# Optimization experiments

Hardware: AMD Instinct MI355X
Metric: run time of the kernel (lower is better)

## Reference

```python
import jax, jax.numpy as jnp
import numpy as np

B, N = 1, 512
C_S, C_Z, C_HID, H, P_Q, P_V = 384, 128, 16, 12, 4, 8
W_C = (2.0 / (9.0 * P_Q)) ** 0.5
W_L = (1.0 / 3.0) ** 0.5
F_IN = H * C_Z + H * C_HID + H * P_V * 3 + H * P_V  # 2112


def setup_inputs() -> dict:
    key = jax.random.key(0)
    ks = jax.random.split(key, 14)
    s_i = jax.random.normal(ks[0], (B, N, C_S), jnp.float32)
    z_ij = jax.random.normal(ks[1], (B, N, N, C_Z), jnp.float32)
    # proper rotation matrices via QR so invert_apply is a true rigid inverse
    rot, _ = jnp.linalg.qr(jax.random.normal(ks[2], (B, N, 3, 3), jnp.float32))
    trans = jax.random.normal(ks[3], (B, N, 3), jnp.float32)
    sc = lambda fan: 1.0 / np.sqrt(fan)
    Wq = jax.random.normal(ks[4], (C_S, H, C_HID), jnp.float32) * sc(C_S)
    Wk = jax.random.normal(ks[5], (C_S, H, C_HID), jnp.float32) * sc(C_S)
    Wv = jax.random.normal(ks[6], (C_S, H, C_HID), jnp.float32) * sc(C_S)
    Wqp = jax.random.normal(ks[7], (C_S, H, P_Q, 3), jnp.float32) * sc(C_S)
    Wkp = jax.random.normal(ks[8], (C_S, H, P_Q, 3), jnp.float32) * sc(C_S)
    Wvp = jax.random.normal(ks[9], (C_S, H, P_V, 3), jnp.float32) * sc(C_S)
    Wb = jax.random.normal(ks[10], (C_Z, H), jnp.float32) * sc(C_Z)
    gamma = jax.random.normal(ks[11], (H,), jnp.float32)
    Wf = jax.random.normal(ks[12], (F_IN, C_S), jnp.float32) * sc(F_IN)
    bf = jnp.zeros((C_S,), jnp.float32)
    return {"s_i": s_i, "z_ij": z_ij, "rot": rot, "trans": trans,
            "Wq": Wq, "Wk": Wk, "Wv": Wv, "Wqp": Wqp, "Wkp": Wkp, "Wvp": Wvp,
            "Wb": Wb, "gamma": gamma, "Wf": Wf, "bf": bf}


def _apply(rot, trans, p):
    # rigid transform per residue: R_i @ p + t_i ; p: (B,N,H,P,3)
    return jnp.einsum('bimn,bihpn->bihpm', rot, p) + trans[:, :, None, None, :]


def reference(s_i, z_ij, rot, trans, Wq, Wk, Wv, Wqp, Wkp, Wvp, Wb, gamma, Wf, bf):
    q = jnp.einsum('bic,chd->bihd', s_i, Wq)            # (B,N,H,C_HID)
    k = jnp.einsum('bic,chd->bihd', s_i, Wk)
    v = jnp.einsum('bic,chd->bihd', s_i, Wv)
    qp = jnp.einsum('bic,chpx->bihpx', s_i, Wqp)        # (B,N,H,Pq,3)
    kp = jnp.einsum('bic,chpx->bihpx', s_i, Wkp)
    vp = jnp.einsum('bic,chpx->bihpx', s_i, Wvp)        # (B,N,H,Pv,3)
    b_ij = jnp.einsum('bijc,ch->bijh', z_ij, Wb)        # pair bias (B,N,N,H)

    qp_g = _apply(rot, trans, qp)
    kp_g = _apply(rot, trans, kp)
    # squared global point distances, summed over points: (B,N,N,H)
    d2 = jnp.sum((qp_g[:, :, None] - kp_g[:, None]) ** 2, axis=(-1, -2))

    qk = jnp.einsum('bihd,bjhd->bijh', q, k) * (1.0 / np.sqrt(C_HID))
    logits = W_L * (qk + b_ij - (W_C * 0.5) * gamma * d2)
    a = jax.nn.softmax(logits, axis=2)                  # softmax over j

    o_pair = jnp.einsum('bijh,bijc->bihc', a, z_ij)     # (B,N,H,C_Z)
    o_sc = jnp.einsum('bijh,bjhd->bihd', a, v)          # (B,N,H,C_HID)
    vp_g = _apply(rot, trans, vp)
    o_pt_g = jnp.einsum('bijh,bjhpx->bihpx', a, vp_g)   # (B,N,H,Pv,3)
    # invert_apply at residue i: R_i^T @ (x - t_i)
    o_pt = jnp.einsum('bimn,bihpm->bihpn', rot, o_pt_g - trans[:, :, None, None, :])
    o_norm = jnp.sqrt(jnp.sum(o_pt ** 2, axis=-1) + 1e-12)  # (B,N,H,Pv)

    feat = jnp.concatenate([o_pair.reshape(B, N, -1), o_sc.reshape(B, N, -1),
                            o_pt.reshape(B, N, -1), o_norm.reshape(B, N, -1)], axis=-1)
    return feat @ Wf + bf
```

## Files before the change

### kernel.cpp

```cpp
#include <hip/hip_runtime.h>
#include <hip/hip_bf16.h>
#include <math.h>

#define Nn    512
#define CS    384
#define CZ    128
#define CH    16
#define Hh    12
#define PQ    4
#define PV    8
#define NCOL  1152
#define FIN   2112

#define W_C   0.23570226039551584f
#define W_L   0.5773502691896258f

typedef unsigned short ushort_t;
typedef unsigned int uint_t;
typedef __attribute__((ext_vector_type(8))) short bf16x8;
typedef __attribute__((ext_vector_type(4))) float f32x4;

#define OFF_P      0u
#define OFF_MQ     589824u
#define OFF_MK     595968u
#define OFF_VT     602112u
#define OFF_VPT    651264u
#define OFF_S16    1830912u
#define OFF_WCT    1929216u
#define OFF_WFT    2150400u
#define OFF_F16    2555904u
#define OFF_PP     3145728u
#define OFF_VFRAG  5328896u
#define OFF_EXT    5451776u
#define OFF_EKB    21755904u
#define OFF_EQB    21854208u
#define OFF_WBF    21952512u

__device__ inline ushort_t f2bf(float f) {
  __hip_bfloat16 h = __float2bfloat16(f);
  return *reinterpret_cast<ushort_t*>(&h);
}
__device__ inline float bf2f(ushort_t u) {
  unsigned int x = ((unsigned int)u) << 16;
  return __uint_as_float(x);
}

__global__ __launch_bounds__(384) void k_conv(
    const float* __restrict__ s, const float* __restrict__ Wq,
    const float* __restrict__ Wk, const float* __restrict__ Wv,
    const float* __restrict__ Wqp, const float* __restrict__ Wkp,
    const float* __restrict__ Wvp, const float* __restrict__ Wf,
    const float* __restrict__ Wb,
    ushort_t* __restrict__ s16, ushort_t* __restrict__ WcatT,
    ushort_t* __restrict__ WfT, ushort_t* __restrict__ wbf) {
  int b = blockIdx.x;
  if (b < 512) {
    int idx = b * 384 + threadIdx.x;
    s16[idx] = f2bf(s[idx]);
  } else if (b < 1664) {
    int col = b - 512, k = threadIdx.x;
    float v;
    if      (col < 192)  v = Wq [k * 192 + col];
    else if (col < 384)  v = Wk [k * 192 + col - 192];
    else if (col < 576)  v = Wv [k * 192 + col - 384];
    else if (col < 720)  v = Wqp[k * 144 + col - 576];
    else if (col < 864)  v = Wkp[k * 144 + col - 720];
    else                 v = Wvp[k * 288 + col - 864];
    WcatT[(size_t)col * CS + k] = f2bf(v);
  } else if (b < 2048) {
    int o = b - 1664;
    for (int f = threadIdx.x; f < FIN; f += 384)
      WfT[(size_t)o * FIN + f] = f2bf(Wf[(size_t)f * CS + o]);
  } else {
    int t = threadIdx.x;
    if (t < 256) {
      int kk = t >> 6, l = t & 63;
      int h = l & 15, lk = l >> 4;
#pragma unroll
      for (int e = 0; e < 8; ++e) {
        int c = kk * 32 + lk * 8 + e;
        wbf[t * 8 + e] = (h < Hh) ? f2bf(Wb[c * Hh + h]) : (ushort_t)0;
      }
    }
  }
}

__global__ __launch_bounds__(64) void k_projm(
    const ushort_t* __restrict__ s16, const ushort_t* __restrict__ WcatT,
    float* __restrict__ P) {
  int colt = blockIdx.x;
  int i0 = blockIdx.y * 16;
  int l = threadIdx.x;
  int cl = l & 15, lk = l >> 4;
  f32x4 accA = {0.f, 0.f, 0.f, 0.f}, accB = {0.f, 0.f, 0.f, 0.f};
  const ushort_t* arow = s16 + (size_t)(i0 + cl) * CS;
  const ushort_t* brow = WcatT + (size_t)(colt * 16 + cl) * CS;
#pragma unroll
  for (int kk = 0; kk < 12; kk += 2) {
    bf16x8 a0 = *(const bf16x8*)(arow + kk * 32 + lk * 8);
    bf16x8 b0 = *(const bf16x8*)(brow + kk * 32 + lk * 8);
    accA = __builtin_amdgcn_mfma_f32_16x16x32_bf16(a0, b0, accA, 0, 0, 0);
    bf16x8 a1 = *(const bf16x8*)(arow + (kk + 1) * 32 + lk * 8);
    bf16x8 b1 = *(const bf16x8*)(brow + (kk + 1) * 32 + lk * 8);
    accB = __builtin_amdgcn_mfma_f32_16x16x32_bf16(a1, b1, accB, 0, 0, 0);
  }
#pragma unroll
  for (int r = 0; r < 4; ++r)
    P[(size_t)(i0 + lk * 4 + r) * NCOL + colt * 16 + cl] = accA[r] + accB[r];
}

__global__ __launch_bounds__(64) void k_prep(
    const float* __restrict__ P, const float* __restrict__ rot,
    const float* __restrict__ trans, const float* __restrict__ gamma,
    ushort_t* __restrict__ eqb, ushort_t* __restrict__ ekb,
    float* __restrict__ mq, float* __restrict__ mk,
    ushort_t* __restrict__ vT, ushort_t* __restrict__ vpT) {
  int gid = blockIdx.x * 64 + threadIdx.x;
  int i = gid / Hh, h = gid % Hh;
  const float* Pi = P + (size_t)i * NCOL;
  float R[9], T[3];
#pragma unroll
  for (int m = 0; m < 9; ++m) R[m] = rot[i * 9 + m];
#pragma unroll
  for (int m = 0; m < 3; ++m) T[m] = trans[i * 3 + m];
  float cg = W_C * gamma[h];

  ushort_t* eq = eqb + (size_t)gid * 32;
  ushort_t* ek = ekb + (size_t)gid * 32;
#pragma unroll
  for (int d = 0; d < CH; ++d) eq[d] = f2bf(Pi[h * CH + d] * 0.25f);
#pragma unroll
  for (int d = 0; d < CH; ++d) ek[d] = f2bf(Pi[192 + h * CH + d]);
  float sq = 0.f, sk = 0.f;
#pragma unroll
  for (int p = 0; p < PQ; ++p) {
    float x = Pi[576 + h * 12 + p * 3 + 0];
    float y = Pi[576 + h * 12 + p * 3 + 1];
    float zc = Pi[576 + h * 12 + p * 3 + 2];
    float gx = R[0] * x + R[1] * y + R[2] * zc + T[0];
    float gy = R[3] * x + R[4] * y + R[5] * zc + T[1];
    float gz = R[6] * x + R[7] * y + R[8] * zc + T[2];
    eq[16 + p * 3 + 0] = f2bf(cg * gx);
    eq[16 + p * 3 + 1] = f2bf(cg * gy);
    eq[16 + p * 3 + 2] = f2bf(cg * gz);
    sq += gx * gx + gy * gy + gz * gz;
  }
#pragma unroll
  for (int p = 0; p < PQ; ++p) {
    float x = Pi[720 + h * 12 + p * 3 + 0];
    float y = Pi[720 + h * 12 + p * 3 + 1];
    float zc = Pi[720 + h * 12 + p * 3 + 2];
    float gx = R[0] * x + R[1] * y + R[2] * zc + T[0];
    float gy = R[3] * x + R[4] * y + R[5] * zc + T[1];
    float gz = R[6] * x + R[7] * y + R[8] * zc + T[2];
    ek[16 + p * 3 + 0] = f2bf(gx);
    ek[16 + p * 3 + 1] = f2bf(gy);
    ek[16 + p * 3 + 2] = f2bf(gz);
    sk += gx * gx + gy * gy + gz * gz;
  }
#pragma unroll
  for (int d = 28; d < 32; ++d) { eq[d] = 0; ek[d] = 0; }
  mq[gid] = -0.5f * cg * sq;
  mk[gid] = -0.5f * cg * sk;

#pragma unroll
  for (int d = 0; d < CH; ++d)
    vT[(size_t)(h * CH + d) * Nn + i] = f2bf(Pi[384 + h * CH + d]);
#pragma unroll
  for (int p = 0; p < PV; ++p) {
    float x = Pi[864 + h * 24 + p * 3 + 0];
    float y = Pi[864 + h * 24 + p * 3 + 1];
    float zc = Pi[864 + h * 24 + p * 3 + 2];
    vpT[(size_t)(h * 24 + p * 3 + 0) * Nn + i] = f2bf(R[0] * x + R[1] * y + R[2] * zc + T[0]);
    vpT[(size_t)(h * 24 + p * 3 + 1) * Nn + i] = f2bf(R[3] * x + R[4] * y + R[5] * zc + T[1]);
    vpT[(size_t)(h * 24 + p * 3 + 2) * Nn + i] = f2bf(R[6] * x + R[7] * y + R[8] * zc + T[2]);
  }
}

__global__ __launch_bounds__(64) void k_vfrag(
    const ushort_t* __restrict__ vT, const ushort_t* __restrict__ vpT,
    ushort_t* __restrict__ vfrag) {
  int tt = blockIdx.x;
  int jb = blockIdx.y;
  int l = threadIdx.x;
  int cl = l & 15, lk = l >> 4;
  const ushort_t* src = (tt < 12)
      ? vT  + (size_t)(tt * 16 + cl) * Nn
      : vpT + (size_t)((tt - 12) * 16 + cl) * Nn;
  bf16x8 v = *(const bf16x8*)(src + jb * 32 + lk * 8);
  *(bf16x8*)(vfrag + (((size_t)tt * 16 + jb) * 64 + l) * 8) = v;
}

__global__ __launch_bounds__(768) void k_ext(
    const ushort_t* __restrict__ eqb, const ushort_t* __restrict__ ekb,
    const float* __restrict__ mk, float* __restrict__ ext) {
  int it = blockIdx.x, jt = blockIdx.y;
  int tid = threadIdx.x;
  int l = tid & 63, h = tid >> 6;
  int cl = l & 15, lk = l >> 4;
  bf16x8 a = *(const bf16x8*)(eqb + ((size_t)(it * 16 + cl) * Hh + h) * 32 + lk * 8);
  bf16x8 b = *(const bf16x8*)(ekb + ((size_t)(jt * 16 + cl) * Hh + h) * 32 + lk * 8);
  f32x4 dl = {0.f, 0.f, 0.f, 0.f};
  dl = __builtin_amdgcn_mfma_f32_16x16x32_bf16(a, b, dl, 0, 0, 0);
  float mkv = mk[(jt * 16 + cl) * Hh + h];
  float* erow = ext + ((size_t)h * Nn + it * 16 + lk * 4) * Nn + jt * 16 + cl;
#pragma unroll
  for (int r = 0; r < 4; ++r) erow[(size_t)r * Nn] = dl[r] + mkv;
}

__global__ __launch_bounds__(512, 4) void k_fused8(
    const float* __restrict__ z, const ushort_t* __restrict__ wbf,
    const float* __restrict__ ext, const ushort_t* __restrict__ vfrag,
    float* __restrict__ pp) {
  __shared__ float smemf[19728];
  char*   ztc  = (char*)smemf;
  float*  extb = smemf + 16384;
  char*   pB   = (char*)(smemf + 16384);
  float*  mb   = smemf + 19456;
  float*  lb   = smemf + 19584;
  float*  Mv   = smemf + 19712;

  int i = blockIdx.x, half = blockIdx.y, tid = threadIdx.x;
  int l = tid & 63, w = tid >> 6;
  int cl = l & 15, lk = l >> 4;
  int j0b = half * 256;
  float* po = pp + ((size_t)i * 2 + half) * 2048;
  int swz = (cl & 7) << 4;

  const float4* zg4 = (const float4*)(z + ((size_t)i * Nn + j0b) * CZ);
  float4 xv0 = zg4[0 * 512 + tid],  xv1 = zg4[1 * 512 + tid];
  float4 xv2 = zg4[2 * 512 + tid],  xv3 = zg4[3 * 512 + tid];
  float4 xv4 = zg4[4 * 512 + tid],  xv5 = zg4[5 * 512 + tid];
  float4 xv6 = zg4[6 * 512 + tid],  xv7 = zg4[7 * 512 + tid];
  float4 xv8 = zg4[8 * 512 + tid],  xv9 = zg4[9 * 512 + tid];
  float4 xv10 = zg4[10 * 512 + tid], xv11 = zg4[11 * 512 + tid];
  float4 xv12 = zg4[12 * 512 + tid], xv13 = zg4[13 * 512 + tid];
  float4 xv14 = zg4[14 * 512 + tid], xv15 = zg4[15 * 512 + tid];
  float ev[6];
#pragma unroll
  for (int q = 0; q < 6; ++q) {
    int idx = q * 512 + tid;
    ev[q] = ext[((size_t)(idx >> 8) * Nn + i) * Nn + j0b + (idx & 255)];
  }

#define STORE_ZT(it_, xv_) { \
    int idx = (it_) * 512 + tid; \
    int row = idx >> 5, c4 = idx & 31; \
    uint2 pk; \
    pk.x = (uint_t)f2bf(xv_.x) | ((uint_t)f2bf(xv_.y) << 16); \
    pk.y = (uint_t)f2bf(xv_.z) | ((uint_t)f2bf(xv_.w) << 16); \
    *(uint2*)&ztc[row * 256 + ((c4 * 8) ^ ((row & 7) << 4))] = pk; }
  STORE_ZT(0, xv0)   STORE_ZT(1, xv1)   STORE_ZT(2, xv2)   STORE_ZT(3, xv3)
  STORE_ZT(4, xv4)   STORE_ZT(5, xv5)   STORE_ZT(6, xv6)   STORE_ZT(7, xv7)
  STORE_ZT(8, xv8)   STORE_ZT(9, xv9)   STORE_ZT(10, xv10) STORE_ZT(11, xv11)
  STORE_ZT(12, xv12) STORE_ZT(13, xv13) STORE_ZT(14, xv14) STORE_ZT(15, xv15)
#undef STORE_ZT
#pragma unroll
  for (int q = 0; q < 6; ++q) {
    int idx = q * 512 + tid;
    extb[(idx & 255) * 12 + (idx >> 8)] = ev[q];
  }
  __syncthreads();

  bf16x8 wbreg[4];
#pragma unroll
  for (int kk = 0; kk < 4; ++kk)
    wbreg[kk] = *(const bf16x8*)&wbf[(kk * 64 + l) * 8];

  float v[2][4];
#pragma unroll
  for (int cg = 0; cg < 2; ++cg) {
    int jloc = w * 32 + cg * 16 + cl;
    f32x4 dl = {0.f, 0.f, 0.f, 0.f};
#pragma unroll
    for (int kk = 0; kk < 4; ++kk) {
      bf16x8 a = *(const bf16x8*)&ztc[jloc * 256 + ((kk * 64 + lk * 16) ^ ((cl & 7) << 4))];
      dl = __builtin_amdgcn_mfma_f32_16x16x32_bf16(a, wbreg[kk], dl, 0, 0, 0);
    }
    if (cl < Hh) {
#pragma unroll
      for (int r = 0; r < 4; ++r)
        v[cg][r] = W_L * (dl[r] + extb[(w * 32 + cg * 16 + lk * 4 + r) * 12 + cl]);
    } else {
#pragma unroll
      for (int r = 0; r < 4; ++r) v[cg][r] = -1e30f;
    }
  }
  __syncthreads();

  float m_w = v[0][0];
#pragma unroll
  for (int cg = 0; cg < 2; ++cg)
#pragma unroll
    for (int r = 0; r < 4; ++r) m_w = fmaxf(m_w, v[cg][r]);
  m_w = fmaxf(m_w, __shfl_xor(m_w, 16));
  m_w = fmaxf(m_w, __shfl_xor(m_w, 32));

  float ps = 0.f;
#pragma unroll
  for (int cg = 0; cg < 2; ++cg) {
    int j = w * 32 + cg * 16 + lk * 4;
    ushort_t p0 = f2bf(__expf(v[cg][0] - m_w));
    ushort_t p1 = f2bf(__expf(v[cg][1] - m_w));
    ushort_t p2 = f2bf(__expf(v[cg][2] - m_w));
    ushort_t p3 = f2bf(__expf(v[cg][3] - m_w));
    ps += bf2f(p0) + bf2f(p1) + bf2f(p2) + bf2f(p3);
    uint2 d;
    d.x = (uint_t)p0 | ((uint_t)p1 << 16);
    d.y = (uint_t)p2 | ((uint_t)p3 << 16);
    *(uint2*)&pB[(cl * 512 + j * 2) ^ swz] = d;
  }
  ps += __shfl_xor(ps, 16);
  ps += __shfl_xor(ps, 32);
  if (lk == 0) { mb[w * 16 + cl] = m_w; lb[w * 16 + cl] = ps; }
  __syncthreads();

  if (tid < 16) {
    float M = mb[tid];
#pragma unroll
    for (int ww = 1; ww < 8; ++ww) M = fmaxf(M, mb[ww * 16 + tid]);
    float L = 0.f;
#pragma unroll
    for (int ww = 0; ww < 8; ++ww) L += lb[ww * 16 + tid] * __expf(mb[ww * 16 + tid] - M);
    Mv[tid] = M;
    po[2016 + tid] = M;
    po[2032 + tid] = L;
  }
  __syncthreads();

  float sf = __expf(m_w - Mv[cl]);
#pragma unroll
  for (int q = 0; q < 2; ++q) {
    int j = w * 32 + lk * 8 + q * 4;
    uint_t off = (uint_t)(cl * 512 + j * 2) ^ swz;
    uint2 d = *(uint2*)&pB[off];
    ushort_t q0 = f2bf(bf2f((ushort_t)(d.x & 0xffff)) * sf);
    ushort_t q1 = f2bf(bf2f((ushort_t)(d.x >> 16)) * sf);
    ushort_t q2 = f2bf(bf2f((ushort_t)(d.y & 0xffff)) * sf);
    ushort_t q3 = f2bf(bf2f((ushort_t)(d.y >> 16)) * sf);
    d.x = (uint_t)q0 | ((uint_t)q1 << 16);
    d.y = (uint_t)q2 | ((uint_t)q3 << 16);
    *(uint2*)&pB[off] = d;
  }
  __syncthreads();

  f32x4 acc[5];
#pragma unroll
  for (int n = 0; n < 5; ++n) acc[n] = (f32x4){0.f, 0.f, 0.f, 0.f};
  bf16x8 vA[4], vB[4];

#define LOADV(buf, kk_) { \
    _Pragma("unroll") \
    for (int n = 1; n < 5; ++n) { \
      int t = w + n * 8; \
      if (t < 38) buf[n - 1] = *(const bf16x8*)(vfrag + \
          (((size_t)(t - 8) * 16 + (half * 8 + (kk_))) * 64 + l) * 8); \
    } }
#define COMPUTE(buf, kk_) { \
    int koff = (kk_) * 32 + lk * 8; \
    bf16x8 af = *(const bf16x8*)&pB[(cl * 512 + koff * 2) ^ swz]; \
    bf16x8 b0; \
    _Pragma("unroll") \
    for (int e = 0; e < 8; ++e) \
      b0[e] = *(const short*)&ztc[(koff + e) * 256 + ((w * 32 + cl * 2) ^ (e << 4))]; \
    acc[0] = __builtin_amdgcn_mfma_f32_16x16x32_bf16(af, b0, acc[0], 0, 0, 0); \
    _Pragma("unroll") \
    for (int n = 1; n < 5; ++n) { \
      int t = w + n * 8; \
      if (t < 38) acc[n] = __builtin_amdgcn_mfma_f32_16x16x32_bf16(af, buf[n - 1], acc[n], 0, 0, 0); \
    } }

  LOADV(vA, 0)
#pragma unroll
  for (int kk = 0; kk < 8; kk += 2) {
    LOADV(vB, kk + 1)
    COMPUTE(vA, kk)
    if (kk < 6) LOADV(vA, kk + 2)
    COMPUTE(vB, kk + 1)
  }
#undef LOADV
#undef COMPUTE

#pragma unroll
  for (int n = 0; n < 5; ++n) {
    int t = w + n * 8;
    if (t < 38) {
      if (t < 8) {
        int c = t * 16 + cl;
#pragma unroll
        for (int r = 0; r < 4; ++r) {
          int h = lk * 4 + r;
          if (h < Hh) po[h * CZ + c] = acc[n][r];
        }
      } else if (t < 20) {
        int h = t - 8;
        if (lk == (h >> 2)) po[1536 + h * CH + cl] = acc[n][h & 3];
      } else {
        int cp = (t - 20) * 16 + cl;
        int h = cp / 24;
        if (lk == (h >> 2)) po[1728 + cp] = acc[n][h & 3];
      }
    }
  }
}

__global__ __launch_bounds__(256) void k_merge(
    const float* __restrict__ pp, const float* __restrict__ rot,
    const float* __restrict__ trans, ushort_t* __restrict__ feat16) {
  __shared__ float a0s[16], a1s[16];
  __shared__ float optg[288];
  int i = blockIdx.x, tid = threadIdx.x;
  const float* p0 = pp + ((size_t)i * 2 + 0) * 2048;
  const float* p1 = pp + ((size_t)i * 2 + 1) * 2048;
  ushort_t* Fi = feat16 + (size_t)i * FIN;

  if (tid < 16) {
    float m0 = p0[2016 + tid], m1 = p1[2016 + tid];
    float M = fmaxf(m0, m1);
    float s0 = __expf(m0 - M), s1 = __expf(m1 - M);
    float L = p0[2032 + tid] * s0 + p1[2032 + tid] * s1;
    float inv = (tid < Hh) ? 1.f / L : 0.f;
    a0s[tid] = s0 * inv;
    a1s[tid] = s1 * inv;
  }
  __syncthreads();

  for (int idx = tid; idx < 1728; idx += 256) {
    int h = (idx < 1536) ? (idx >> 7) : ((idx - 1536) >> 4);
    Fi[idx] = f2bf(p0[idx] * a0s[h] + p1[idx] * a1s[h]);
  }
  for (int idx = tid; idx < 288; idx += 256) {
    int h = idx / 24;
    optg[idx] = p0[1728 + idx] * a0s[h] + p1[1728 + idx] * a1s[h];
  }
  __syncthreads();

  if (tid < 96) {
    int h = tid >> 3, p = tid & 7;
    int cp = h * 24 + p * 3;
    float g0 = optg[cp + 0] - trans[i * 3 + 0];
    float g1 = optg[cp + 1] - trans[i * 3 + 1];
    float g2 = optg[cp + 2] - trans[i * 3 + 2];
    const float* R = rot + i * 9;
    float ss = 0.f;
#pragma unroll
    for (int nn2 = 0; nn2 < 3; ++nn2) {
      float o = R[nn2] * g0 + R[3 + nn2] * g1 + R[6 + nn2] * g2;
      Fi[1728 + cp + nn2] = f2bf(o);
      ss += o * o;
    }
    Fi[2016 + h * 8 + p] = f2bf(sqrtf(ss + 1e-12f));
  }
}

__global__ __launch_bounds__(256) void k_outm2(
    const ushort_t* __restrict__ feat16, const ushort_t* __restrict__ WfT,
    const float* __restrict__ bfv, float* __restrict__ out) {
  __shared__ f32x4 red[4][64];
  int ot = blockIdx.x;
  int ib = blockIdx.y;
  int tid = threadIdx.x;
  int l = tid & 63, w = tid >> 6;
  int cl = l & 15, lk = l >> 4;
  int i0 = ib * 32 + (w >> 1) * 16;
  int kw = w & 1;
  const ushort_t* arow = feat16 + (size_t)(i0 + cl) * FIN;
  const ushort_t* brow = WfT + (size_t)(ot * 16 + cl) * FIN;
  f32x4 accA = {0.f, 0.f, 0.f, 0.f}, accB = {0.f, 0.f, 0.f, 0.f};
  int k0 = kw * 33;
#pragma unroll 4
  for (int kk = k0; kk < k0 + 32; kk += 2) {
    bf16x8 a0 = *(const bf16x8*)(arow + kk * 32 + lk * 8);
    bf16x8 b0 = *(const bf16x8*)(brow + kk * 32 + lk * 8);
    accA = __builtin_amdgcn_mfma_f32_16x16x32_bf16(a0, b0, accA, 0, 0, 0);
    bf16x8 a1 = *(const bf16x8*)(arow + (kk + 1) * 32 + lk * 8);
    bf16x8 b1 = *(const bf16x8*)(brow + (kk + 1) * 32 + lk * 8);
    accB = __builtin_amdgcn_mfma_f32_16x16x32_bf16(a1, b1, accB, 0, 0, 0);
  }
  {
    int kk = k0 + 32;
    bf16x8 a = *(const bf16x8*)(arow + kk * 32 + lk * 8);
    bf16x8 b = *(const bf16x8*)(brow + kk * 32 + lk * 8);
    accA = __builtin_amdgcn_mfma_f32_16x16x32_bf16(a, b, accA, 0, 0, 0);
  }
#pragma unroll
  for (int r = 0; r < 4; ++r) accA[r] += accB[r];
  red[w][l] = accA;
  __syncthreads();
  if (kw == 0) {
    f32x4 s = red[w][l];
    f32x4 o = red[w + 1][l];
    float bias = bfv[ot * 16 + cl];
#pragma unroll
    for (int r = 0; r < 4; ++r)
      out[(size_t)(i0 + lk * 4 + r) * CS + ot * 16 + cl] = s[r] + o[r] + bias;
  }
}

extern "C" void kernel_launch(void* const* d_in, const int* in_sizes, int n_in,
                              void* d_out, int out_size, void* d_ws, size_t ws_size,
                              hipStream_t stream) {
  const float* s_i   = (const float*)d_in[0];
  const float* z_ij  = (const float*)d_in[1];
  const float* rot   = (const float*)d_in[2];
  const float* trans = (const float*)d_in[3];
  const float* Wq    = (const float*)d_in[4];
  const float* Wk    = (const float*)d_in[5];
  const float* Wv    = (const float*)d_in[6];
  const float* Wqp   = (const float*)d_in[7];
  const float* Wkp   = (const float*)d_in[8];
  const float* Wvp   = (const float*)d_in[9];
  const float* Wb    = (const float*)d_in[10];
  const float* gamma = (const float*)d_in[11];
  const float* Wf    = (const float*)d_in[12];
  const float* bf    = (const float*)d_in[13];
  float* out = (float*)d_out;

  float* w = (float*)d_ws;
  float*    P     = w + OFF_P;
  float*    mq    = w + OFF_MQ;
  float*    mk    = w + OFF_MK;
  ushort_t* vT    = (ushort_t*)(w + OFF_VT);
  ushort_t* vpT   = (ushort_t*)(w + OFF_VPT);
  ushort_t* s16   = (ushort_t*)(w + OFF_S16);
  ushort_t* WcT   = (ushort_t*)(w + OFF_WCT);
  ushort_t* WfT   = (ushort_t*)(w + OFF_WFT);
  ushort_t* f16   = (ushort_t*)(w + OFF_F16);
  float*    pp    = w + OFF_PP;
  ushort_t* vfrag = (ushort_t*)(w + OFF_VFRAG);
  float*    ext   = w + OFF_EXT;
  ushort_t* ekb   = (ushort_t*)(w + OFF_EKB);
  ushort_t* eqb   = (ushort_t*)(w + OFF_EQB);
  ushort_t* wbf   = (ushort_t*)(w + OFF_WBF);

  k_conv<<<2049, 384, 0, stream>>>(s_i, Wq, Wk, Wv, Wqp, Wkp, Wvp, Wf, Wb,
                                   s16, WcT, WfT, wbf);
  k_projm<<<dim3(72, 32), 64, 0, stream>>>(s16, WcT, P);
  k_prep<<<96, 64, 0, stream>>>(P, rot, trans, gamma, eqb, ekb, mq, mk, vT, vpT);
  k_vfrag<<<dim3(30, 16), 64, 0, stream>>>(vT, vpT, vfrag);
  k_ext<<<dim3(32, 32), 768, 0, stream>>>(eqb, ekb, mk, ext);
  k_fused8<<<dim3(512, 2), 512, 0, stream>>>(z_ij, wbf, ext, vfrag, pp);
  k_merge<<<512, 256, 0, stream>>>(pp, rot, trans, f16);
  k_outm2<<<dim3(24, 16), 256, 0, stream>>>(f16, WfT, bf, out);
}
```

Baseline: 94.09 us.

## Merge ext and vfrag kernels; make fused-kernel preload wave-local to drop barriers

The two small prep kernels (the ext logit tile MFMA and the vfrag repack) are combined into one launch, which saves one kernel launch and its gap. In the main fused kernel each wave now loads only its own 32 rows of z and ext, so the two block-wide barriers around staging can be removed. The ext staging buffer is moved to its own shared-memory region and stored as bf16. This adds rounding error to the logits and slightly more LDS use, which could affect occupancy.

Result: faster. 89.27 us, median of 2 (-5.1%).

```diff
diff --git a/kernel.cpp b/kernel.cpp
--- a/kernel.cpp
+++ b/kernel.cpp
@@ -177,48 +177,51 @@
   }
 }
 
-__global__ __launch_bounds__(64) void k_vfrag(
+__global__ __launch_bounds__(768) void k_aux(
+    const ushort_t* __restrict__ eqb, const ushort_t* __restrict__ ekb,
+    const float* __restrict__ mk, float* __restrict__ ext,
     const ushort_t* __restrict__ vT, const ushort_t* __restrict__ vpT,
     ushort_t* __restrict__ vfrag) {
-  int tt = blockIdx.x;
-  int jb = blockIdx.y;
-  int l = threadIdx.x;
-  int cl = l & 15, lk = l >> 4;
-  const ushort_t* src = (tt < 12)
-      ? vT  + (size_t)(tt * 16 + cl) * Nn
-      : vpT + (size_t)((tt - 12) * 16 + cl) * Nn;
-  bf16x8 v = *(const bf16x8*)(src + jb * 32 + lk * 8);
-  *(bf16x8*)(vfrag + (((size_t)tt * 16 + jb) * 64 + l) * 8) = v;
-}
-
-__global__ __launch_bounds__(768) void k_ext(
-    const ushort_t* __restrict__ eqb, const ushort_t* __restrict__ ekb,
-    const float* __restrict__ mk, float* __restrict__ ext) {
-  int it = blockIdx.x, jt = blockIdx.y;
-  int tid = threadIdx.x;
-  int l = tid & 63, h = tid >> 6;
-  int cl = l & 15, lk = l >> 4;
-  bf16x8 a = *(const bf16x8*)(eqb + ((size_t)(it * 16 + cl) * Hh + h) * 32 + lk * 8);
-  bf16x8 b = *(const bf16x8*)(ekb + ((size_t)(jt * 16 + cl) * Hh + h) * 32 + lk * 8);
-  f32x4 dl = {0.f, 0.f, 0.f, 0.f};
-  dl = __builtin_amdgcn_mfma_f32_16x16x32_bf16(a, b, dl, 0, 0, 0);
-  float mkv = mk[(jt * 16 + cl) * Hh + h];
-  float* erow = ext + ((size_t)h * Nn + it * 16 + lk * 4) * Nn + jt * 16 + cl;
-#pragma unroll
-  for (int r = 0; r < 4; ++r) erow[(size_t)r * Nn] = dl[r] + mkv;
-}
-
-__global__ __launch_bounds__(512, 4) void k_fused8(
+  int b = blockIdx.x, tid = threadIdx.x;
+  if (b < 1024) {
+    int it = b >> 5, jt = b & 31;
+    int l = tid & 63, h = tid >> 6;
+    int cl = l & 15, lk = l >> 4;
+    bf16x8 a = *(const bf16x8*)(eqb + ((size_t)(it * 16 + cl) * Hh + h) * 32 + lk * 8);
+    bf16x8 bb = *(const bf16x8*)(ekb + ((size_t)(jt * 16 + cl) * Hh + h) * 32 + lk * 8);
+    f32x4 dl = {0.f, 0.f, 0.f, 0.f};
+    dl = __builtin_amdgcn_mfma_f32_16x16x32_bf16(a, bb, dl, 0, 0, 0);
+    float mkv = mk[(jt * 16 + cl) * Hh + h];
+    float* erow = ext + ((size_t)h * Nn + it * 16 + lk * 4) * Nn + jt * 16 + cl;
+#pragma unroll
+    for (int r = 0; r < 4; ++r) erow[(size_t)r * Nn] = dl[r] + mkv;
+  } else {
+    int flat = (b - 1024) * 768 + tid;
+    if (flat < 30720) {
+      int tt = flat >> 10;
+      int r = flat & 1023;
+      int jb = r >> 6, l = r & 63;
+      int cl = l & 15, lk = l >> 4;
+      const ushort_t* src = (tt < 12)
+          ? vT  + (size_t)(tt * 16 + cl) * Nn
+          : vpT + (size_t)((tt - 12) * 16 + cl) * Nn;
+      bf16x8 v = *(const bf16x8*)(src + jb * 32 + lk * 8);
+      *(bf16x8*)(vfrag + (((size_t)tt * 16 + jb) * 64 + l) * 8) = v;
+    }
+  }
+}
+
+__global__ __launch_bounds__(512, 4) void k_fused9(
     const float* __restrict__ z, const ushort_t* __restrict__ wbf,
     const float* __restrict__ ext, const ushort_t* __restrict__ vfrag,
     float* __restrict__ pp) {
-  __shared__ float smemf[19728];
-  char*   ztc  = (char*)smemf;
-  float*  extb = smemf + 16384;
-  char*   pB   = (char*)(smemf + 16384);
-  float*  mb   = smemf + 19456;
-  float*  lb   = smemf + 19584;
-  float*  Mv   = smemf + 19712;
+  __shared__ float smemf[20240];
+  char*     ztc  = (char*)smemf;
+  char*     pB   = (char*)smemf + 65536;
+  ushort_t* extb = (ushort_t*)((char*)smemf + 73728);
+  float*    mb   = smemf + 19968;
+  float*    lb   = smemf + 20096;
+  float*    Mv   = smemf + 20224;
 
   int i = blockIdx.x, half = blockIdx.y, tid = threadIdx.x;
   int l = tid & 63, w = tid >> 6;
@@ -228,24 +231,25 @@
   int swz = (cl & 7) << 4;
 
   const float4* zg4 = (const float4*)(z + ((size_t)i * Nn + j0b) * CZ);
-  float4 xv0 = zg4[0 * 512 + tid],  xv1 = zg4[1 * 512 + tid];
-  float4 xv2 = zg4[2 * 512 + tid],  xv3 = zg4[3 * 512 + tid];
-  float4 xv4 = zg4[4 * 512 + tid],  xv5 = zg4[5 * 512 + tid];
-  float4 xv6 = zg4[6 * 512 + tid],  xv7 = zg4[7 * 512 + tid];
-  float4 xv8 = zg4[8 * 512 + tid],  xv9 = zg4[9 * 512 + tid];
-  float4 xv10 = zg4[10 * 512 + tid], xv11 = zg4[11 * 512 + tid];
-  float4 xv12 = zg4[12 * 512 + tid], xv13 = zg4[13 * 512 + tid];
-  float4 xv14 = zg4[14 * 512 + tid], xv15 = zg4[15 * 512 + tid];
+  float4 xv0 = zg4[w * 1024 + 0 * 64 + l],  xv1 = zg4[w * 1024 + 1 * 64 + l];
+  float4 xv2 = zg4[w * 1024 + 2 * 64 + l],  xv3 = zg4[w * 1024 + 3 * 64 + l];
+  float4 xv4 = zg4[w * 1024 + 4 * 64 + l],  xv5 = zg4[w * 1024 + 5 * 64 + l];
+  float4 xv6 = zg4[w * 1024 + 6 * 64 + l],  xv7 = zg4[w * 1024 + 7 * 64 + l];
+  float4 xv8 = zg4[w * 1024 + 8 * 64 + l],  xv9 = zg4[w * 1024 + 9 * 64 + l];
+  float4 xv10 = zg4[w * 1024 + 10 * 64 + l], xv11 = zg4[w * 1024 + 11 * 64 + l];
+  float4 xv12 = zg4[w * 1024 + 12 * 64 + l], xv13 = zg4[w * 1024 + 13 * 64 + l];
+  float4 xv14 = zg4[w * 1024 + 14 * 64 + l], xv15 = zg4[w * 1024 + 15 * 64 + l];
   float ev[6];
 #pragma unroll
   for (int q = 0; q < 6; ++q) {
-    int idx = q * 512 + tid;
-    ev[q] = ext[((size_t)(idx >> 8) * Nn + i) * Nn + j0b + (idx & 255)];
+    int flat = q * 64 + l;
+    int eh = flat >> 5, ejl = flat & 31;
+    ev[q] = ext[((size_t)eh * Nn + i) * Nn + j0b + w * 32 + ejl];
   }
 
 #define STORE_ZT(it_, xv_) { \
-    int idx = (it_) * 512 + tid; \
-    int row = idx >> 5, c4 = idx & 31; \
+    int idxl = (it_) * 64 + l; \
+    int row = w * 32 + (idxl >> 5), c4 = idxl & 31; \
     uint2 pk; \
     pk.x = (uint_t)f2bf(xv_.x) | ((uint_t)f2bf(xv_.y) << 16); \
     pk.y = (uint_t)f2bf(xv_.z) | ((uint_t)f2bf(xv_.w) << 16); \
@@ -257,10 +261,9 @@
 #undef STORE_ZT
 #pragma unroll
   for (int q = 0; q < 6; ++q) {
-    int idx = q * 512 + tid;
-    extb[(idx & 255) * 12 + (idx >> 8)] = ev[q];
-  }
-  __syncthreads();
+    int flat = q * 64 + l;
+    extb[(w * 32 + (flat & 31)) * 12 + (flat >> 5)] = f2bf(ev[q]);
+  }
 
   bf16x8 wbreg[4];
 #pragma unroll
@@ -280,13 +283,13 @@
     if (cl < Hh) {
 #pragma unroll
       for (int r = 0; r < 4; ++r)
-        v[cg][r] = W_L * (dl[r] + extb[(w * 32 + cg * 16 + lk * 4 + r) * 12 + cl]);
+        v[cg][r] = W_L * (dl[r] +
+            bf2f(extb[(w * 32 + cg * 16 + lk * 4 + r) * 12 + cl]));
     } else {
 #pragma unroll
       for (int r = 0; r < 4; ++r) v[cg][r] = -1e30f;
     }
   }
-  __syncthreads();
 
   float m_w = v[0][0];
 #pragma unroll
@@ -537,9 +540,8 @@
                                    s16, WcT, WfT, wbf);
   k_projm<<<dim3(72, 32), 64, 0, stream>>>(s16, WcT, P);
   k_prep<<<96, 64, 0, stream>>>(P, rot, trans, gamma, eqb, ekb, mq, mk, vT, vpT);
-  k_vfrag<<<dim3(30, 16), 64, 0, stream>>>(vT, vpT, vfrag);
-  k_ext<<<dim3(32, 32), 768, 0, stream>>>(eqb, ekb, mk, ext);
-  k_fused8<<<dim3(512, 2), 512, 0, stream>>>(z_ij, wbf, ext, vfrag, pp);
+  k_aux<<<1064, 768, 0, stream>>>(eqb, ekb, mk, ext, vT, vpT, vfrag);
+  k_fused9<<<dim3(512, 2), 512, 0, stream>>>(z_ij, wbf, ext, vfrag, pp);
   k_merge<<<512, 256, 0, stream>>>(pp, rot, trans, f16);
   k_outm2<<<dim3(24, 16), 256, 0, stream>>>(f16, WfT, bf, out);
 }
```
